# Kernel tuning notes

Hardware: AMD Instinct MI355X
Metric: run time of the kernel (lower is better)

## Reference

```python
import jax, jax.numpy as jnp
import numpy as np

B, S, D = 2, 2048, 1024
H = 16
DH = D // H  # 64


def setup_inputs() -> dict:
    key = jax.random.key(0)
    k1, k2, k3 = jax.random.split(key, 3)
    X = jax.random.normal(k1, (B, S, D), dtype=jnp.float32)
    # xavier_normal for Linear(D, 3*D): std = sqrt(2/(fan_in+fan_out))
    std_qkv = float(np.sqrt(2.0 / (D + 3 * D)))
    std_out = float(np.sqrt(2.0 / (D + D)))
    W_qkv = jax.random.normal(k2, (3 * H * DH, D), dtype=jnp.float32) * std_qkv
    W_out = jax.random.normal(k3, (D, H * DH), dtype=jnp.float32) * std_out
    return {"X": X, "W_qkv": W_qkv, "W_out": W_out}


def reference(X, W_qkv, W_out):
    b, s, d = X.shape
    # stacked projection: (b, s, 3*H*DH), then per-head chunk into q,k,v
    qkv = jnp.einsum('bsd,ed->bse', X, W_qkv)
    qkv = qkv.reshape(b, s, H, 3 * DH)
    q, k, v = jnp.split(qkv, 3, axis=-1)  # each (b, s, H, DH)
    scale = 1.0 / jnp.sqrt(jnp.asarray(DH, dtype=X.dtype))
    # naive unfused attention: full [b,H,s,s] score matrix
    scores = jnp.einsum('bqhd,bkhd->bhqk', q, k) * scale
    attn = jax.nn.softmax(scores, axis=-1)
    vals = jnp.einsum('bhqk,bkhd->bqhd', attn, v)
    vals = vals.reshape(b, s, H * DH)
    out = jnp.einsum('bse,de->bsd', vals, W_out)
    return out
```

## Files before the change

kernel.cpp:

```cpp
#include <hip/hip_runtime.h>
#include <cstdint>
#include <cstddef>

typedef __bf16 bf16;
typedef __bf16 bf16x8 __attribute__((ext_vector_type(8)));
typedef __bf16 bf16x2 __attribute__((ext_vector_type(2)));
typedef float  floatx4 __attribute__((ext_vector_type(4)));

typedef __attribute__((address_space(1))) void gvoid_t;
typedef __attribute__((address_space(3))) void lvoid_t;

#define MFMA16(a, b, c) __builtin_amdgcn_mfma_f32_16x16x32_bf16((a), (b), (c), 0, 0, 0)

#if __has_builtin(__builtin_amdgcn_exp2f)
#define EXP2(x) __builtin_amdgcn_exp2f(x)
#else
#define EXP2(x) exp2f(x)
#endif

#define S_TOK 2048
#define E3 3072
#define DMODEL 1024

#define NX 4194304
#define NWQ 3145728
#define NWO 1048576
__global__ __launch_bounds__(256) void cvt_all(const float* __restrict__ X,
                                               const float* __restrict__ Wq,
                                               const float* __restrict__ Wo,
                                               bf16* __restrict__ Xb,
                                               bf16* __restrict__ Wqb,
                                               bf16* __restrict__ Wob) {
  int i = (blockIdx.x * 256 + threadIdx.x) * 8;
  const float* s;
  bf16* d;
  float sc = 1.0f;
  int off;
  if (i < NX) {
    s = X; d = Xb; off = i;
  } else if (i < NX + NWQ) {
    off = i - NX; s = Wq; d = Wqb;
    int row = off >> 10;
    if ((row % 192) < 64) sc = 0.18033688011f;
  } else {
    off = i - NX - NWQ; s = Wo; d = Wob;
  }
  const float4* p = (const float4*)(s + off);
  float4 a = p[0], b = p[1];
  bf16x8 o;
  o[0] = (bf16)(a.x * sc); o[1] = (bf16)(a.y * sc);
  o[2] = (bf16)(a.z * sc); o[3] = (bf16)(a.w * sc);
  o[4] = (bf16)(b.x * sc); o[5] = (bf16)(b.y * sc);
  o[6] = (bf16)(b.z * sc); o[7] = (bf16)(b.w * sc);
  *(bf16x8*)(d + off) = o;
}

__device__ __forceinline__ void gl_lds16(const bf16* g, bf16* l) {
  __builtin_amdgcn_global_load_lds((gvoid_t*)g, (lvoid_t*)l, 16, 0, 0);
}

template <bool OUT_BF16, bool FUSE_V>
__global__ __launch_bounds__(256) void gemm_bt(const bf16* __restrict__ A,
                                               const bf16* __restrict__ Bt,
                                               void* __restrict__ Cv,
                                               bf16* __restrict__ Vt,
                                               int M, int N, int K) {
  __shared__ bf16 sA[128 * 64];
  __shared__ bf16 sB[128 * 64];
  const int tid = threadIdx.x;
  const int wv = tid >> 6, lane = tid & 63;
  const int wr = wv >> 1, wc = wv & 1;
  const int lrow = lane & 15, lgrp = lane >> 4;
  const int R0 = blockIdx.y * 128, C0 = blockIdx.x * 128;

  floatx4 acc[4][4] = {};

  const int srow = lane >> 3;
  const int schk = (lane & 7) ^ srow;
  const bf16* gA = A + (size_t)(R0 + wv * 32 + srow) * K + schk * 8;
  const bf16* gB = Bt + (size_t)(C0 + wv * 32 + srow) * K + schk * 8;
  bf16* lA = sA + wv * 32 * 64;
  bf16* lB = sB + wv * 32 * 64;
  const size_t rs8 = (size_t)8 * K;

  for (int k0 = 0; k0 < K; k0 += 64) {
#pragma unroll
    for (int c = 0; c < 4; c++) {
      gl_lds16(gA + k0 + c * rs8, lA + c * 512);
      gl_lds16(gB + k0 + c * rs8, lB + c * 512);
    }
    __syncthreads();
#pragma unroll
    for (int kk = 0; kk < 2; kk++) {
      bf16x8 af[4], bfr[4];
#pragma unroll
      for (int i = 0; i < 4; i++) {
        int r = wr * 64 + i * 16 + lrow;
        af[i] = *(const bf16x8*)&sA[r * 64 + ((kk * 4 + lgrp) ^ (r & 7)) * 8];
      }
#pragma unroll
      for (int j = 0; j < 4; j++) {
        int r = wc * 64 + j * 16 + lrow;
        bfr[j] = *(const bf16x8*)&sB[r * 64 + ((kk * 4 + lgrp) ^ (r & 7)) * 8];
      }
#pragma unroll
      for (int i = 0; i < 4; i++)
#pragma unroll
        for (int j = 0; j < 4; j++)
          acc[i][j] = MFMA16(af[i], bfr[j], acc[i][j]);
    }
    __syncthreads();
  }

  const int rbase = R0 + wr * 64 + lgrp * 4;
  const int cbase = C0 + wc * 64 + lrow;
  if (OUT_BF16) {
    bf16* C = (bf16*)Cv;
#pragma unroll
    for (int i = 0; i < 4; i++)
#pragma unroll
      for (int j = 0; j < 4; j++) {
        const int col = cbase + j * 16;
        const int m192 = col % 192;
        const int hh = col / 192;
#pragma unroll
        for (int r = 0; r < 4; r++) {
          const int row = rbase + i * 16 + r;
          bf16 val = (bf16)acc[i][j][r];
          bf16* dst;
          if (FUSE_V && m192 >= 128) {
            const int sl = row & 2047;
            const int sp = (sl & ~31) | ((sl & 15) << 1) | ((sl >> 4) & 1);
            dst = Vt + ((size_t)(((row >> 11) * 16 + hh) * 64 + (m192 - 128))) * S_TOK + sp;
          } else {
            dst = C + (size_t)row * N + col;
          }
          *dst = val;
        }
      }
  } else {
    float* C = (float*)Cv;
#pragma unroll
    for (int i = 0; i < 4; i++)
#pragma unroll
      for (int j = 0; j < 4; j++)
#pragma unroll
        for (int r = 0; r < 4; r++)
          C[(size_t)(rbase + i * 16 + r) * N + cbase + j * 16] = acc[i][j][r];
  }
}

__global__ __launch_bounds__(256) void gemm_bt_n64(const bf16* __restrict__ A,
                                                   const bf16* __restrict__ Bt,
                                                   float* __restrict__ C,
                                                   int M, int N, int K) {
  __shared__ bf16 sA[128 * 64];
  __shared__ bf16 sB[64 * 64];
  const int tid = threadIdx.x;
  const int wv = tid >> 6, lane = tid & 63;
  const int wr = wv >> 1, wc = wv & 1;
  const int lrow = lane & 15, lgrp = lane >> 4;
  const int R0 = blockIdx.y * 128, C0 = blockIdx.x * 64;

  floatx4 acc[4][2] = {};

  const int srow = lane >> 3;
  const int schk = (lane & 7) ^ srow;
  const bf16* gA = A + (size_t)(R0 + wv * 32 + srow) * K + schk * 8;
  const bf16* gB = Bt + (size_t)(C0 + wv * 16 + srow) * K + schk * 8;
  bf16* lA = sA + wv * 32 * 64;
  bf16* lB = sB + wv * 16 * 64;
  const size_t rs8 = (size_t)8 * K;

  for (int k0 = 0; k0 < K; k0 += 64) {
#pragma unroll
    for (int c = 0; c < 4; c++) gl_lds16(gA + k0 + c * rs8, lA + c * 512);
#pragma unroll
    for (int c = 0; c < 2; c++) gl_lds16(gB + k0 + c * rs8, lB + c * 512);
    __syncthreads();
#pragma unroll
    for (int kk = 0; kk < 2; kk++) {
      bf16x8 af[4], bfr[2];
#pragma unroll
      for (int i = 0; i < 4; i++) {
        int r = wr * 64 + i * 16 + lrow;
        af[i] = *(const bf16x8*)&sA[r * 64 + ((kk * 4 + lgrp) ^ (r & 7)) * 8];
      }
#pragma unroll
      for (int j = 0; j < 2; j++) {
        int r = wc * 32 + j * 16 + lrow;
        bfr[j] = *(const bf16x8*)&sB[r * 64 + ((kk * 4 + lgrp) ^ (r & 7)) * 8];
      }
#pragma unroll
      for (int i = 0; i < 4; i++)
#pragma unroll
        for (int j = 0; j < 2; j++)
          acc[i][j] = MFMA16(af[i], bfr[j], acc[i][j]);
    }
    __syncthreads();
  }

  const int rbase = R0 + wr * 64 + lgrp * 4;
  const int cbase = C0 + wc * 32 + lrow;
#pragma unroll
  for (int i = 0; i < 4; i++)
#pragma unroll
    for (int j = 0; j < 2; j++)
#pragma unroll
      for (int r = 0; r < 4; r++)
        C[(size_t)(rbase + i * 16 + r) * N + cbase + j * 16] = acc[i][j][r];
}

__global__ __launch_bounds__(512, 2) void attn(const bf16* __restrict__ qkv,
                                               const bf16* __restrict__ Vt,
                                               bf16* __restrict__ vals) {
  __shared__ bf16 sK[2][128 * 64];
  __shared__ bf16 sV[2][64 * 128];
  __shared__ bf16 sP[8][2][2][640];

  const int tid = threadIdx.x;
  const int wv = tid >> 6, lane = tid & 63;
  const int lrow = lane & 15, lgrp = lane >> 4;
  const int b = blockIdx.z, h = blockIdx.x;
  const int qb = blockIdx.y * 256;

  const int srow = lane >> 3;
  const int scol = (lane & 7) ^ srow;
  const bf16* kg0 = qkv + (size_t)(b * S_TOK + wv * 8 + srow) * E3 + h * 192 + 64 + scol * 8;
  const int vrow = lane >> 4;
  const int vchk = lane & 15;
  const int d0 = wv * 8 + vrow, d1 = d0 + 4;
  const bf16* vg0 = Vt + (size_t)((b * 16 + h) * 64 + d0) * S_TOK + (vchk ^ (d0 & 15)) * 8;
  const bf16* vg1 = Vt + (size_t)((b * 16 + h) * 64 + d1) * S_TOK + (vchk ^ (d1 & 15)) * 8;

  const bf16* qp = qkv + (size_t)(b * S_TOK + qb + wv * 32) * E3 + h * 192;
  bf16x8 qa[2][2];
#pragma unroll
  for (int rt = 0; rt < 2; rt++)
#pragma unroll
    for (int dh = 0; dh < 2; dh++)
      qa[rt][dh] = *(const bf16x8*)(qp + (size_t)(rt * 16 + lrow) * E3 + dh * 32 + lgrp * 8);

  floatx4 O[2][4] = {};
  floatx4 lacc[2] = {};
  floatx4 sc[2][2];
  bf16x8 ones;
  const bf16 one1 = (bf16)1.0f;
#pragma unroll
  for (int j = 0; j < 8; j++) ones[j] = one1;

  auto stage = [&](int buf, int st) {
    const bf16* kg = kg0 + (size_t)st * 128 * E3;
    gl_lds16(kg, &sK[buf][wv * 512]);
    gl_lds16(kg + (size_t)64 * E3, &sK[buf][4096 + wv * 512]);
    gl_lds16(vg0 + st * 128, &sV[buf][wv * 1024]);
    gl_lds16(vg1 + st * 128, &sV[buf][wv * 1024 + 512]);
  };

  auto qk_g = [&](int buf, int g) {
    bf16x8 kf[2][2];
#pragma unroll
    for (int t = 0; t < 2; t++)
#pragma unroll
      for (int dh = 0; dh < 2; dh++)
        kf[t][dh] = *(const bf16x8*)&sK[buf][(g * 32 + t * 16 + lrow) * 64 +
                                            ((dh * 4 + lgrp) ^ (lrow & 7)) * 8];
    __builtin_amdgcn_s_setprio(1);
#pragma unroll
    for (int rt = 0; rt < 2; rt++) {
      floatx4 a0 = {0.f, 0.f, 0.f, 0.f}, a1 = {0.f, 0.f, 0.f, 0.f};
      a0 = MFMA16(qa[rt][0], kf[0][0], a0);
      a0 = MFMA16(qa[rt][1], kf[0][1], a0);
      a1 = MFMA16(qa[rt][0], kf[1][0], a1);
      a1 = MFMA16(qa[rt][1], kf[1][1], a1);
      sc[rt][0] = a0;
      sc[rt][1] = a1;
    }
    __builtin_amdgcn_s_setprio(0);
  };

  auto expw_g = [&](int g) {
#pragma unroll
    for (int rt = 0; rt < 2; rt++)
#pragma unroll
      for (int r = 0; r < 4; r++) {
        bf16x2 h2;
        h2[0] = (bf16)EXP2(sc[rt][0][r]);
        h2[1] = (bf16)EXP2(sc[rt][1][r]);
        *(unsigned*)&sP[wv][rt][g & 1][(lgrp * 4 + r) * 40 + lrow * 2] =
            __builtin_bit_cast(unsigned, h2);
      }
  };

  auto pv_g = [&](int buf, int g) {
    bf16x8 vf[4];
#pragma unroll
    for (int dt = 0; dt < 4; dt++)
      vf[dt] = *(const bf16x8*)&sV[buf][(dt * 16 + lrow) * 128 + ((g * 4 + lgrp) ^ lrow) * 8];
    __builtin_amdgcn_s_setprio(1);
#pragma unroll
    for (int rt = 0; rt < 2; rt++) {
      bf16x8 pf = *(const bf16x8*)&sP[wv][rt][g & 1][lrow * 40 + lgrp * 8];
#pragma unroll
      for (int dt = 0; dt < 4; dt++) O[rt][dt] = MFMA16(pf, vf[dt], O[rt][dt]);
      lacc[rt] = MFMA16(pf, ones, lacc[rt]);
    }
    __builtin_amdgcn_s_setprio(0);
  };

  auto compute = [&](int buf) {
    qk_g(buf, 0); expw_g(0);
    qk_g(buf, 1); expw_g(1);
    pv_g(buf, 0);
    qk_g(buf, 2); expw_g(2);
    pv_g(buf, 1);
    qk_g(buf, 3); expw_g(3);
    pv_g(buf, 2);
    pv_g(buf, 3);
  };

  stage(0, 0);
  __syncthreads();
#pragma unroll 1
  for (int st = 0; st < 16; st += 2) {
    stage(1, st + 1);
    compute(0);
    __syncthreads();
    if (st + 2 < 16) stage(0, st + 2);
    compute(1);
    __syncthreads();
  }

  bf16* vout = vals + (size_t)(b * S_TOK + qb + wv * 32) * DMODEL + h * 64;
#pragma unroll
  for (int rt = 0; rt < 2; rt++)
#pragma unroll
    for (int r = 0; r < 4; r++) {
      float rinv = __builtin_amdgcn_rcpf(lacc[rt][r]);
#pragma unroll
      for (int dt = 0; dt < 4; dt++)
        vout[(size_t)(rt * 16 + lgrp * 4 + r) * DMODEL + dt * 16 + lrow] =
            (bf16)(O[rt][dt][r] * rinv);
    }
}

extern "C" void kernel_launch(void* const* d_in, const int* in_sizes, int n_in,
                              void* d_out, int out_size, void* d_ws, size_t ws_size,
                              hipStream_t stream) {
  const float* X = (const float*)d_in[0];
  const float* Wqkv = (const float*)d_in[1];
  const float* Wout = (const float*)d_in[2];
  float* out = (float*)d_out;

  char* ws = (char*)d_ws;
  bf16* Xb = (bf16*)(ws);
  bf16* Wqb = (bf16*)(ws + ((size_t)8 << 20));
  bf16* Wob = (bf16*)(ws + ((size_t)14 << 20));
  bf16* qkvb = (bf16*)(ws + ((size_t)16 << 20));
  bf16* Vt = (bf16*)(ws + ((size_t)40 << 20));
  bf16* vals = (bf16*)(ws + ((size_t)48 << 20));

  cvt_all<<<(NX + NWQ + NWO) / 2048, 256, 0, stream>>>(X, Wqkv, Wout, Xb, Wqb, Wob);

  gemm_bt<true, true><<<dim3(24, 32), 256, 0, stream>>>(Xb, Wqb, qkvb, Vt, 4096, 3072, 1024);

  attn<<<dim3(16, 8, 2), 512, 0, stream>>>(qkvb, Vt, vals);

  gemm_bt_n64<<<dim3(16, 32), 256, 0, stream>>>(vals, Wob, out, 4096, 1024, 1024);
}
```

Baseline: 178.9 us.

## Keep softmax probabilities in registers via transposed QK MFMA and V permutation

Computes scores as K·Q^T so each lane holds a column of probabilities. The probabilities then feed the PV MFMA operand directly through a register bpermute, with no round trip through shared memory. The V-transpose store permutation in the QKV GEMM epilogue changes so the key ordering matches this new register layout. The row sum now comes from lane-local adds plus cross-lane shuffles instead of an extra MFMA against a ones vector. This removes the LDS writes and reads for P and one MFMA per tile, at the cost of bpermute traffic and tighter coupling between the V layout and the attention kernel.

Measured after the change: 171.6 us. 1.04x faster.

```diff
diff --git a/kernel.cpp b/kernel.cpp
--- a/kernel.cpp
+++ b/kernel.cpp
@@ -6,6 +6,7 @@
 typedef __bf16 bf16x8 __attribute__((ext_vector_type(8)));
 typedef __bf16 bf16x2 __attribute__((ext_vector_type(2)));
 typedef float  floatx4 __attribute__((ext_vector_type(4)));
+typedef unsigned uintx4 __attribute__((ext_vector_type(4)));
 
 typedef __attribute__((address_space(1))) void gvoid_t;
 typedef __attribute__((address_space(3))) void lvoid_t;
@@ -130,7 +131,11 @@
           bf16* dst;
           if (FUSE_V && m192 >= 128) {
             const int sl = row & 2047;
-            const int sp = (sl & ~31) | ((sl & 15) << 1) | ((sl >> 4) & 1);
+            const int sl5 = sl & 31;
+            int q5;
+            if (sl5 < 16) q5 = ((sl5 >> 2) << 3) | (sl5 & 3);
+            else q5 = (((((sl5 >> 2) & 3) ^ 2) << 3) | 4) | (sl5 & 3);
+            const int sp = (sl & ~31) | q5;
             dst = Vt + ((size_t)(((row >> 11) * 16 + hh) * 64 + (m192 - 128))) * S_TOK + sp;
           } else {
             dst = C + (size_t)row * N + col;
@@ -216,7 +221,6 @@
                                                bf16* __restrict__ vals) {
   __shared__ bf16 sK[2][128 * 64];
   __shared__ bf16 sV[2][64 * 128];
-  __shared__ bf16 sP[8][2][2][640];
 
   const int tid = threadIdx.x;
   const int wv = tid >> 6, lane = tid & 63;
@@ -242,12 +246,8 @@
       qa[rt][dh] = *(const bf16x8*)(qp + (size_t)(rt * 16 + lrow) * E3 + dh * 32 + lgrp * 8);
 
   floatx4 O[2][4] = {};
-  floatx4 lacc[2] = {};
-  floatx4 sc[2][2];
-  bf16x8 ones;
-  const bf16 one1 = (bf16)1.0f;
-#pragma unroll
-  for (int j = 0; j < 8; j++) ones[j] = one1;
+  float lsum[2] = {0.f, 0.f};
+  const int xaddr = (lane ^ 32) << 2;
 
   auto stage = [&](int buf, int st) {
     const bf16* kg = kg0 + (size_t)st * 128 * E3;
@@ -257,7 +257,7 @@
     gl_lds16(vg1 + st * 128, &sV[buf][wv * 1024 + 512]);
   };
 
-  auto qk_g = [&](int buf, int g) {
+  auto qk_g = [&](int buf, int g, floatx4 (&sc)[2][2]) {
     bf16x8 kf[2][2];
 #pragma unroll
     for (int t = 0; t < 2; t++)
@@ -269,30 +269,39 @@
 #pragma unroll
     for (int rt = 0; rt < 2; rt++) {
       floatx4 a0 = {0.f, 0.f, 0.f, 0.f}, a1 = {0.f, 0.f, 0.f, 0.f};
-      a0 = MFMA16(qa[rt][0], kf[0][0], a0);
-      a0 = MFMA16(qa[rt][1], kf[0][1], a0);
-      a1 = MFMA16(qa[rt][0], kf[1][0], a1);
-      a1 = MFMA16(qa[rt][1], kf[1][1], a1);
+      a0 = MFMA16(kf[0][0], qa[rt][0], a0);
+      a0 = MFMA16(kf[0][1], qa[rt][1], a0);
+      a1 = MFMA16(kf[1][0], qa[rt][0], a1);
+      a1 = MFMA16(kf[1][1], qa[rt][1], a1);
       sc[rt][0] = a0;
       sc[rt][1] = a1;
     }
     __builtin_amdgcn_s_setprio(0);
   };
 
-  auto expw_g = [&](int g) {
-#pragma unroll
-    for (int rt = 0; rt < 2; rt++)
-#pragma unroll
-      for (int r = 0; r < 4; r++) {
-        bf16x2 h2;
-        h2[0] = (bf16)EXP2(sc[rt][0][r]);
-        h2[1] = (bf16)EXP2(sc[rt][1][r]);
-        *(unsigned*)&sP[wv][rt][g & 1][(lgrp * 4 + r) * 40 + lrow * 2] =
-            __builtin_bit_cast(unsigned, h2);
-      }
-  };
-
-  auto pv_g = [&](int buf, int g) {
+  auto sm_g = [&](floatx4 (&sc)[2][2], unsigned (&pfw)[2][4]) {
+#pragma unroll
+    for (int rt = 0; rt < 2; rt++) {
+      float e0 = EXP2(sc[rt][0][0]), e1 = EXP2(sc[rt][0][1]);
+      float e2 = EXP2(sc[rt][0][2]), e3 = EXP2(sc[rt][0][3]);
+      float e4 = EXP2(sc[rt][1][0]), e5 = EXP2(sc[rt][1][1]);
+      float e6 = EXP2(sc[rt][1][2]), e7 = EXP2(sc[rt][1][3]);
+      lsum[rt] += ((e0 + e1) + (e2 + e3)) + ((e4 + e5) + (e6 + e7));
+      bf16x2 w;
+      w[0] = (bf16)e0; w[1] = (bf16)e1;
+      pfw[rt][0] = __builtin_bit_cast(unsigned, w);
+      w[0] = (bf16)e2; w[1] = (bf16)e3;
+      pfw[rt][1] = __builtin_bit_cast(unsigned, w);
+      w[0] = (bf16)e4; w[1] = (bf16)e5;
+      unsigned t10 = __builtin_bit_cast(unsigned, w);
+      w[0] = (bf16)e6; w[1] = (bf16)e7;
+      unsigned t11 = __builtin_bit_cast(unsigned, w);
+      pfw[rt][2] = (unsigned)__builtin_amdgcn_ds_bpermute(xaddr, (int)t10);
+      pfw[rt][3] = (unsigned)__builtin_amdgcn_ds_bpermute(xaddr, (int)t11);
+    }
+  };
+
+  auto pv_g = [&](int buf, int g, unsigned (&pfw)[2][4]) {
     bf16x8 vf[4];
 #pragma unroll
     for (int dt = 0; dt < 4; dt++)
@@ -300,23 +309,22 @@
     __builtin_amdgcn_s_setprio(1);
 #pragma unroll
     for (int rt = 0; rt < 2; rt++) {
-      bf16x8 pf = *(const bf16x8*)&sP[wv][rt][g & 1][lrow * 40 + lgrp * 8];
+      uintx4 pw = {pfw[rt][0], pfw[rt][1], pfw[rt][2], pfw[rt][3]};
+      bf16x8 pf = __builtin_bit_cast(bf16x8, pw);
 #pragma unroll
       for (int dt = 0; dt < 4; dt++) O[rt][dt] = MFMA16(pf, vf[dt], O[rt][dt]);
-      lacc[rt] = MFMA16(pf, ones, lacc[rt]);
     }
     __builtin_amdgcn_s_setprio(0);
   };
 
   auto compute = [&](int buf) {
-    qk_g(buf, 0); expw_g(0);
-    qk_g(buf, 1); expw_g(1);
-    pv_g(buf, 0);
-    qk_g(buf, 2); expw_g(2);
-    pv_g(buf, 1);
-    qk_g(buf, 3); expw_g(3);
-    pv_g(buf, 2);
-    pv_g(buf, 3);
+    floatx4 scA[2][2], scB[2][2];
+    unsigned pfA[2][4], pfB[2][4];
+    qk_g(buf, 0, scA); sm_g(scA, pfA);
+    qk_g(buf, 1, scB); sm_g(scB, pfB); pv_g(buf, 0, pfA);
+    qk_g(buf, 2, scA); sm_g(scA, pfA); pv_g(buf, 1, pfB);
+    qk_g(buf, 3, scB); sm_g(scB, pfB); pv_g(buf, 2, pfA);
+    pv_g(buf, 3, pfB);
   };
 
   stage(0, 0);
@@ -331,12 +339,19 @@
     __syncthreads();
   }
 
+#pragma unroll
+  for (int rt = 0; rt < 2; rt++) {
+    lsum[rt] += __shfl_xor(lsum[rt], 16);
+    lsum[rt] += __shfl_xor(lsum[rt], 32);
+  }
+
   bf16* vout = vals + (size_t)(b * S_TOK + qb + wv * 32) * DMODEL + h * 64;
 #pragma unroll
   for (int rt = 0; rt < 2; rt++)
 #pragma unroll
     for (int r = 0; r < 4; r++) {
-      float rinv = __builtin_amdgcn_rcpf(lacc[rt][r]);
+      float rs = __shfl(lsum[rt], lgrp * 4 + r);
+      float rinv = __builtin_amdgcn_rcpf(rs);
 #pragma unroll
       for (int dt = 0; dt < 4; dt++)
         vout[(size_t)(rt * 16 + lgrp * 4 + r) * DMODEL + dt * 16 + lrow] =
```
